# Kernel optimization log

Measured on AMD Instinct MI355X. Metric: run time of the kernel, lower is better.

Reference implementation:

```python
import jax, jax.numpy as jnp
import numpy as np

V = 10000   # vocab (input and output)
E = 128     # embed dim
H = 256     # hidden dim (encoder == decoder, required for shapes to work)
B = 64      # batch
S = 128     # src len
T = 64      # trg len


def setup_inputs() -> dict:
    key = jax.random.key(0)
    ks = jax.random.split(key, 24)
    sc = 0.05
    rn = lambda k, shp: jax.random.normal(k, shp, jnp.float32) * sc
    inp = {
        "src": jax.random.randint(ks[0], (B, S), 0, V),
        "trg": jax.random.randint(ks[1], (B, T), 0, V),
        "tf_mask": jnp.ones((T,), bool),  # True -> teacher forcing at that step
        # encoder params
        "enc_emb": rn(ks[2], (V, E)),
        "e1f_Wih": rn(ks[3], (4 * H, E)), "e1f_Whh": rn(ks[4], (4 * H, H)), "e1f_b": rn(ks[5], (4 * H,)),
        "e1b_Wih": rn(ks[6], (4 * H, E)), "e1b_Whh": rn(ks[7], (4 * H, H)), "e1b_b": rn(ks[8], (4 * H,)),
        "e2f_Wih": rn(ks[9], (4 * H, 2 * H)), "e2f_Whh": rn(ks[10], (4 * H, H)), "e2f_b": rn(ks[11], (4 * H,)),
        "e2b_Wih": rn(ks[12], (4 * H, 2 * H)), "e2b_Whh": rn(ks[13], (4 * H, H)), "e2b_b": rn(ks[14], (4 * H,)),
        # decoder params
        "dec_emb": rn(ks[15], (V, E)),
        "Wa": rn(ks[16], (H, 3 * H)), "ba": rn(ks[17], (H,)), "v": rn(ks[18], (H,)),
        "dWih": rn(ks[19], (4 * H, E + 2 * H)), "db": rn(ks[20], (4 * H,)),
        "Wfc": rn(ks[21], (V, 3 * H)), "bfc": rn(ks[22], (V,)),
    }
    return inp


def _lstm_dir(x, Wih, Whh, b, reverse):
    # x: [B, S, Din] -> hidden seq [B, S, H]; torch gate order i,f,g,o
    h0 = jnp.zeros((x.shape[0], Whh.shape[1]), x.dtype)

    def step(carry, xt):
        h, c = carry
        g = xt @ Wih.T + h @ Whh.T + b
        i, f, gg, o = jnp.split(g, 4, axis=-1)
        c = jax.nn.sigmoid(f) * c + jax.nn.sigmoid(i) * jnp.tanh(gg)
        h = jax.nn.sigmoid(o) * jnp.tanh(c)
        return (h, c), h

    _, hs = jax.lax.scan(step, (h0, h0), jnp.swapaxes(x, 0, 1), reverse=reverse)
    return jnp.swapaxes(hs, 0, 1)


def _bilstm(x, fW, fU, fb, bW, bU, bb):
    return jnp.concatenate([_lstm_dir(x, fW, fU, fb, False),
                            _lstm_dir(x, bW, bU, bb, True)], axis=-1)


def _seq2seq(src, trg, tf_mask, enc_emb,
             e1f_Wih, e1f_Whh, e1f_b, e1b_Wih, e1b_Whh, e1b_b,
             e2f_Wih, e2f_Whh, e2f_b, e2b_Wih, e2b_Whh, e2b_b,
             dec_emb, Wa, ba, v, dWih, db, Wfc, bfc):
    # encoder (dropout in eval mode -> identity)
    emb = enc_emb[src]                                   # [B,S,E]
    out1 = _bilstm(emb, e1f_Wih, e1f_Whh, e1f_b, e1b_Wih, e1b_Whh, e1b_b)   # [B,S,2H]
    enc_out = _bilstm(out1, e2f_Wih, e2f_Whh, e2f_b, e2b_Wih, e2b_Whh, e2b_b)  # [B,S,2H]

    bsz, slen = src.shape
    hidden0 = enc_out[:, -1, :H]                         # forward final state [B,H]

    def step(carry, xs):
        hidden, tok = carry
        trg_t, tf = xs
        embedded = dec_emb[tok]                          # [B,E]
        # Bahdanau attention
        rep = jnp.broadcast_to(hidden[:, None, :], (bsz, slen, H))
        energy = jnp.tanh(jnp.concatenate([rep, enc_out], -1) @ Wa.T + ba)  # [B,S,H]
        attn = jax.nn.softmax(energy @ v, axis=-1)       # [B,S]
        context = jnp.einsum('bs,bsd->bd', attn, enc_out)  # [B,2H]
        # LSTM step with fresh zero (h,c), as in the original (no state threaded)
        xin = jnp.concatenate([embedded, context], -1)   # [B,E+2H]
        g = xin @ dWih.T + db
        i, f, gg, o = jnp.split(g, 4, axis=-1)
        c = jax.nn.sigmoid(i) * jnp.tanh(gg)             # f gate irrelevant with c0=0
        h = jax.nn.sigmoid(o) * jnp.tanh(c)
        pred = jnp.concatenate([h, context], -1) @ Wfc.T + bfc  # [B,V]
        top1 = jnp.argmax(pred, axis=-1)
        nxt = jnp.where(tf, trg_t, top1)
        return (h, nxt), pred

    xs = (jnp.swapaxes(trg[:, 1:], 0, 1), tf_mask[1:])
    _, preds = jax.lax.scan(step, (hidden0, trg[:, 0]), xs)  # [T-1,B,V]
    preds = jnp.swapaxes(preds, 0, 1)                        # [B,T-1,V]
    zero0 = jnp.zeros((bsz, 1, preds.shape[-1]), preds.dtype)
    return jnp.concatenate([zero0, preds], axis=1)           # [B,T,V]


def reference(src, trg, tf_mask, enc_emb,
              e1f_Wih, e1f_Whh, e1f_b, e1b_Wih, e1b_Whh, e1b_b,
              e2f_Wih, e2f_Whh, e2f_b, e2b_Wih, e2b_Whh, e2b_b,
              dec_emb, Wa, ba, v, dWih, db, Wfc, bfc):
    return _seq2seq(src, trg, tf_mask, enc_emb,
                    e1f_Wih, e1f_Whh, e1f_b, e1b_Wih, e1b_Whh, e1b_b,
                    e2f_Wih, e2f_Whh, e2f_b, e2b_Wih, e2b_Whh, e2b_b,
                    dec_emb, Wa, ba, v, dWih, db, Wfc, bfc)
```

## Files before the change

### kernel.cpp

```cpp
#include <hip/hip_runtime.h>
#include <hip/hip_bf16.h>
#include <cstdint>


typedef __hip_bfloat16 bf16;
typedef __attribute__((ext_vector_type(8))) short short8;
typedef __attribute__((ext_vector_type(4))) float f32x4;

#define OFF_E1F_WIH 0L
#define OFF_E1B_WIH 131072L
#define OFF_E2F_WIH 262144L
#define OFF_E2B_WIH 786432L
#define OFF_E1F_WHH 1310720L
#define OFF_E1B_WHH 1572864L
#define OFF_E2F_WHH 1835008L
#define OFF_E2B_WHH 2097152L
#define OFF_DWIH    2359296L
#define OFF_WFC     3014656L
#define OFF_WA      10694656L
#define WBF_TOTAL   10891264L

__device__ __align__(16) bf16     g_WBF[WBF_TOTAL];
__device__ __align__(16) float    g_X1F[8192 * 1024];
__device__ __align__(16) float    g_X1B[8192 * 1024];
__device__ __align__(16) bf16     g_EMB[8192 * 128];
__device__ __align__(16) bf16     g_OUT1[8192 * 512];
__device__ __align__(16) bf16     g_ENC[8192 * 512];
__device__ __align__(16) float    g_EWA[8192 * 256];
__device__ __align__(16) float    g_HID[64 * 256];
__device__ __align__(16) bf16     g_XIN[64 * 640];
__device__ __align__(16) bf16     g_HC[64 * 768];

__device__ __forceinline__ float b2f(bf16 x) { return __bfloat162float(x); }
__device__ __forceinline__ float fexp2(float x) { return __builtin_amdgcn_exp2f(x); }
__device__ __forceinline__ float frcp(float x)  { return __builtin_amdgcn_rcpf(x); }
__device__ __forceinline__ float clampf(float x, float L) {
  return fminf(fmaxf(x, -L), L);
}
__device__ __forceinline__ float sigf(float x) {
  x = clampf(x, 30.f);
  return frcp(1.f + fexp2(-1.44269504f * x));
}
__device__ __forceinline__ float tanh_f(float x) {
  x = clampf(x, 15.f);
  float e = fexp2(2.885390082f * x);
  return (e - 1.f) * frcp(e + 1.f);
}
__device__ __forceinline__ f32x4 mfma16(short8 a, short8 b, f32x4 c) {
  return __builtin_amdgcn_mfma_f32_16x16x32_bf16(a, b, c, 0, 0, 0);
}

__global__ __launch_bounds__(256) void cvt_w(const float* __restrict__ src,
                                             long off, int n) {
  int i = (blockIdx.x * 256 + threadIdx.x) * 4;
  if (i >= n) return;
  float4 v = *(const float4*)(src + i);
  bf16* d = g_WBF + off + i;
  d[0] = __float2bfloat16(v.x);
  d[1] = __float2bfloat16(v.y);
  d[2] = __float2bfloat16(v.z);
  d[3] = __float2bfloat16(v.w);
}

__global__ __launch_bounds__(256) void embed_k(const int* __restrict__ src,
                                               const float* __restrict__ tab) {
  int i4 = (blockIdx.x * 256 + threadIdx.x) * 4;
  int row = i4 >> 7, e = i4 & 127;
  int tok = src[row];
  if (tok < 0 || tok >= 10000) tok = 0;
  float4 v = *(const float4*)&tab[(size_t)tok * 128 + e];
  bf16* d = &g_EMB[(size_t)row * 128 + e];
  d[0] = __float2bfloat16(v.x);
  d[1] = __float2bfloat16(v.y);
  d[2] = __float2bfloat16(v.z);
  d[3] = __float2bfloat16(v.w);
}

__device__ __forceinline__ void gemm_core(const bf16* __restrict__ A, int lda,
                                          const bf16* __restrict__ W, int ldw, int wcol,
                                          const float* __restrict__ bias,
                                          float* __restrict__ Cf,
                                          long ldc, int N, int K, float clampL) {
  const int wave = threadIdx.x >> 6, lane = threadIdx.x & 63;
  const int l15 = lane & 15, quad = lane >> 4;
  const int m0 = blockIdx.x * 64 + wave * 16;
  const int n0 = blockIdx.y * 64;

  f32x4 acc[4];
#pragma unroll
  for (int j = 0; j < 4; ++j) acc[j] = (f32x4){0.f, 0.f, 0.f, 0.f};

  const bf16* Arow = A + (size_t)(m0 + l15) * lda + quad * 8;
  for (int k = 0; k < K; k += 32) {
    short8 a = *(const short8*)(Arow + k);
#pragma unroll
    for (int j = 0; j < 4; ++j) {
      int n = n0 + 16 * j + l15;
      short8 bfr = (short8){0, 0, 0, 0, 0, 0, 0, 0};
      if (n < N) bfr = *(const short8*)(W + (size_t)n * ldw + wcol + k + quad * 8);
      acc[j] = mfma16(a, bfr, acc[j]);
    }
  }
#pragma unroll
  for (int j = 0; j < 4; ++j) {
    int n = n0 + 16 * j + l15;
    if (n >= N) continue;
    float bv = bias ? bias[n] : 0.f;
#pragma unroll
    for (int r = 0; r < 4; ++r) {
      int m = m0 + quad * 4 + r;
      Cf[(size_t)m * ldc + n] = clampf(acc[j][r] + bv, clampL);
    }
  }
}

__global__ __launch_bounds__(256) void gemm_x1(long offW, const float* __restrict__ bias,
                                               int bwd) {
  gemm_core(g_EMB, 128, g_WBF + offW, 128, 0, bias, bwd ? g_X1B : g_X1F,
            1024, 1024, 128, 64.f);
}
__global__ __launch_bounds__(256) void gemm_x2(long offW, const float* __restrict__ bias,
                                               int bwd) {
  gemm_core(g_OUT1, 512, g_WBF + offW, 512, 0, bias, bwd ? g_X1B : g_X1F,
            1024, 1024, 512, 64.f);
}
__global__ __launch_bounds__(256) void gemm_ewa() {
  gemm_core(g_ENC, 512, g_WBF + OFF_WA, 768, 256, nullptr, g_EWA, 256, 256, 512, 64.f);
}
__global__ __launch_bounds__(256) void gemm_pred(const float* __restrict__ bfc,
                                                 float* __restrict__ outp, int step) {
  gemm_core(g_HC, 768, g_WBF + OFF_WFC, 768, 0, bfc, outp + (size_t)step * 10000,
            640000, 10000, 768, 512.f);
}

__global__ __launch_bounds__(512, 2) void lstm_batch(long offWhf, long offWhb,
                                                     int layer) {
  const int bx = blockIdx.x;
  const int d = bx & 1, bg = bx >> 1;
  const int b0 = bg * 16;
  const float* __restrict__ X  = d ? g_X1B : g_X1F;
  const bf16*  __restrict__ Wh = g_WBF + (d ? offWhb : offWhf);
  bf16* __restrict__ out = layer ? g_ENC : g_OUT1;

  __shared__ __align__(16) bf16 hlds[16 * 264];
  __shared__ float gst[16 * 1028];

  const int tid = threadIdx.x;
  const int wave = tid >> 6, lane = tid & 63, l15 = lane & 15, quad = lane >> 4;
  const int n0 = wave * 128;
  const int u  = tid & 255;
  const int bh = tid >> 8;

  short8 bs[4][8];
#pragma unroll
  for (int kt = 0; kt < 4; ++kt)
#pragma unroll
    for (int nt = 0; nt < 8; ++nt)
      bs[kt][nt] = *(const short8*)(Wh + (size_t)(n0 + 16 * nt + l15) * 256 +
                                    kt * 32 + quad * 8);

  for (int i = tid; i < 16 * 264; i += 512) hlds[i] = __float2bfloat16(0.f);
  float creg[8];
#pragma unroll
  for (int i = 0; i < 8; ++i) creg[i] = 0.f;

  float xreg[32];
  {
    const int s0 = d ? 127 : 0;
#pragma unroll
    for (int j = 0; j < 8; ++j) {
      const size_t xr = ((size_t)(b0 + bh * 8 + j) * 128 + s0) * 1024 + u;
#pragma unroll
      for (int g = 0; g < 4; ++g) xreg[j * 4 + g] = X[xr + g * 256];
    }
  }
  __syncthreads();

  const bf16* Wstr = Wh + (size_t)(n0 + l15) * 256 + quad * 8;

  for (int t = 0; t < 128; ++t) {
    const int s = d ? (127 - t) : t;
    f32x4 acc[8];
#pragma unroll
    for (int nt = 0; nt < 8; ++nt) acc[nt] = (f32x4){0.f, 0.f, 0.f, 0.f};

#pragma unroll
    for (int kt = 0; kt < 4; ++kt) {
      short8 a = *(const short8*)&hlds[l15 * 264 + kt * 32 + quad * 8];
#pragma unroll
      for (int nt = 0; nt < 8; ++nt) acc[nt] = mfma16(a, bs[kt][nt], acc[nt]);
    }
#pragma unroll
    for (int kt = 4; kt < 8; ++kt) {
      short8 a = *(const short8*)&hlds[l15 * 264 + kt * 32 + quad * 8];
#pragma unroll
      for (int nt = 0; nt < 8; ++nt) {
        short8 bfr = *(const short8*)(Wstr + (size_t)nt * 16 * 256 + kt * 32);
        acc[nt] = mfma16(a, bfr, acc[nt]);
      }
    }

#pragma unroll
    for (int nt = 0; nt < 8; ++nt) {
      int col = n0 + 16 * nt + l15;
#pragma unroll
      for (int r = 0; r < 4; ++r)
        gst[(quad * 4 + r) * 1028 + col] = clampf(acc[nt][r], 64.f);
    }
    __syncthreads();

#pragma unroll
    for (int j = 0; j < 8; ++j) {
      const int b = bh * 8 + j;
      const int gb = b0 + b;
      float gi = gst[b * 1028 + u]       + xreg[j * 4 + 0];
      float gf = gst[b * 1028 + 256 + u] + xreg[j * 4 + 1];
      float gg = gst[b * 1028 + 512 + u] + xreg[j * 4 + 2];
      float go = gst[b * 1028 + 768 + u] + xreg[j * 4 + 3];
      float c = clampf(sigf(gf) * creg[j] + sigf(gi) * tanh_f(gg), 256.f);
      creg[j] = c;
      float h = clampf(sigf(go) * tanh_f(c), 4.f);
      out[((size_t)gb * 128 + s) * 512 + (size_t)d * 256 + u] = __float2bfloat16(h);
      if (layer == 1 && d == 0 && t == 127)
        g_HID[gb * 256 + u] = h;
      hlds[b * 264 + u] = __float2bfloat16(h);
    }

    {
      const int tn = (t < 127) ? (t + 1) : t;
      const int sn = d ? (127 - tn) : tn;
#pragma unroll
      for (int j = 0; j < 8; ++j) {
        const size_t xr = ((size_t)(b0 + bh * 8 + j) * 128 + sn) * 1024 + u;
#pragma unroll
        for (int g = 0; g < 4; ++g) xreg[j * 4 + g] = X[xr + g * 256];
      }
    }
    __syncthreads();
  }
}

__global__ __launch_bounds__(256) void attn_step(int step,
                                                 const int* __restrict__ trg,
                                                 const unsigned char* __restrict__ tfm,
                                                 const float* __restrict__ dec_emb,
                                                 const float* __restrict__ Wa,
                                                 const float* __restrict__ ba,
                                                 const float* __restrict__ vv,
                                                 const float* __restrict__ outp)
{
  int b = blockIdx.x, tid = threadIdx.x;
  __shared__ float sh[256], hb[256], vsh[256], es[128], red[256];
  __shared__ int ridx[256];
  __shared__ int stok;

  if (step == 1) {
    if (tid == 0) stok = trg[b * 64];
  } else {
    const float* pr = outp + (size_t)b * 640000 + (size_t)(step - 1) * 10000;
    float bv = -3.4e38f; int bi = 0;
    for (int v2 = tid; v2 < 10000; v2 += 256) {
      float pv = pr[v2];
      if (pv > bv) { bv = pv; bi = v2; }
    }
    red[tid] = bv; ridx[tid] = bi;
    __syncthreads();
    for (int off = 128; off; off >>= 1) {
      if (tid < off) {
        float ov = red[tid + off]; int oi = ridx[tid + off];
        if (ov > red[tid] || (ov == red[tid] && oi < ridx[tid])) { red[tid] = ov; ridx[tid] = oi; }
      }
      __syncthreads();
    }
    if (tid == 0) {
      int k = step - 1;
      int tf = (int)tfm[k] | (int)tfm[4 * k];
      int tok = tf ? trg[b * 64 + k] : ridx[0];
      if (tok < 0 || tok >= 10000) tok = 0;
      stok = tok;
    }
    __syncthreads();
  }

  sh[tid]  = g_HID[b * 256 + tid];
  vsh[tid] = vv[tid];
  __syncthreads();

  {
    float acc = 0.f;
    const float* wr = Wa + (size_t)tid * 768;
    for (int k4 = 0; k4 < 256; k4 += 4) {
      float4 w4 = *(const float4*)(wr + k4);
      acc += sh[k4] * w4.x + sh[k4 + 1] * w4.y + sh[k4 + 2] * w4.z + sh[k4 + 3] * w4.w;
    }
    hb[tid] = clampf(acc + ba[tid], 64.f);
  }
  __syncthreads();

  int wv = tid >> 6, ln = tid & 63;
  for (int s = wv; s < 128; s += 4) {
    const float* Er = g_EWA + ((size_t)b * 128 + s) * 256;
    float part = 0.f;
#pragma unroll
    for (int jj = 0; jj < 4; ++jj) {
      int j = ln + 64 * jj;
      part += tanh_f(hb[j] + Er[j]) * vsh[j];
    }
    part += __shfl_down(part, 32);
    part += __shfl_down(part, 16);
    part += __shfl_down(part, 8);
    part += __shfl_down(part, 4);
    part += __shfl_down(part, 2);
    part += __shfl_down(part, 1);
    if (ln == 0) es[s] = clampf(part, 512.f);
  }
  __syncthreads();

  red[tid] = (tid < 128) ? es[tid] : -3.4e38f;
  __syncthreads();
  for (int off = 128; off; off >>= 1) { if (tid < off) red[tid] = fmaxf(red[tid], red[tid + off]); __syncthreads(); }
  float mx = red[0];
  __syncthreads();
  float pexp = (tid < 128) ? fexp2((es[tid] - mx) * 1.44269504f) : 0.f;
  red[tid] = pexp;
  __syncthreads();
  for (int off = 128; off; off >>= 1) { if (tid < off) red[tid] += red[tid + off]; __syncthreads(); }
  float inv = frcp(red[0]);
  __syncthreads();
  if (tid < 128) es[tid] = pexp * inv;
  __syncthreads();

  float c0 = 0.f, c1 = 0.f;
  for (int s = 0; s < 128; ++s) {
    const bf16* er = g_ENC + ((size_t)b * 128 + s) * 512;
    float a = es[s];
    c0 += a * b2f(er[tid]);
    c1 += a * b2f(er[tid + 256]);
  }
  c0 = clampf(c0, 16.f);
  c1 = clampf(c1, 16.f);
  g_XIN[(size_t)b * 640 + 128 + tid] = __float2bfloat16(c0);
  g_XIN[(size_t)b * 640 + 384 + tid] = __float2bfloat16(c1);
  g_HC [(size_t)b * 768 + 256 + tid] = __float2bfloat16(c0);
  g_HC [(size_t)b * 768 + 512 + tid] = __float2bfloat16(c1);
  if (tid < 128)
    g_XIN[(size_t)b * 640 + tid] = __float2bfloat16(dec_emb[(size_t)stok * 128 + tid]);
}

__global__ __launch_bounds__(256) void dec_gemm_cell(const float* __restrict__ db) {
  __shared__ float gst[64 * 68];
  const int tid = threadIdx.x;
  const int wave = tid >> 6, lane = tid & 63, l15 = lane & 15, quad = lane >> 4;
  const int u0 = blockIdx.x * 16;

  f32x4 acc[4];
#pragma unroll
  for (int mt = 0; mt < 4; ++mt) acc[mt] = (f32x4){0.f, 0.f, 0.f, 0.f};

  const bf16* Brow = g_WBF + OFF_DWIH + (size_t)(wave * 256 + u0 + l15) * 640 + quad * 8;
  for (int kt = 0; kt < 20; ++kt) {
    short8 bfr = *(const short8*)(Brow + kt * 32);
#pragma unroll
    for (int mt = 0; mt < 4; ++mt) {
      short8 a = *(const short8*)(g_XIN + (size_t)(16 * mt + l15) * 640 + kt * 32 + quad * 8);
      acc[mt] = mfma16(a, bfr, acc[mt]);
    }
  }
#pragma unroll
  for (int mt = 0; mt < 4; ++mt)
#pragma unroll
    for (int r = 0; r < 4; ++r)
      gst[(16 * mt + quad * 4 + r) * 68 + wave * 16 + l15] = clampf(acc[mt][r], 64.f);
  __syncthreads();

  for (int p = tid; p < 1024; p += 256) {
    int b = p >> 4, uu = p & 15;
    int u = u0 + uu;
    float gi = gst[b * 68 + 0  + uu] + db[u];
    float gg = gst[b * 68 + 32 + uu] + db[512 + u];
    float go = gst[b * 68 + 48 + uu] + db[768 + u];
    float c = sigf(gi) * tanh_f(gg);
    float h = clampf(sigf(go) * tanh_f(c), 4.f);
    g_HID[b * 256 + u] = h;
    g_HC[(size_t)b * 768 + u] = __float2bfloat16(h);
  }
}

__global__ __launch_bounds__(256) void zero_t0(float* __restrict__ outp) {
  int idx = blockIdx.x * 256 + threadIdx.x;
  int b = idx / 10000, v = idx - b * 10000;
  outp[(size_t)b * 640000 + v] = 0.f;
}

extern "C" void kernel_launch(void* const* d_in, const int* in_sizes, int n_in,
                              void* d_out, int out_size, void* d_ws, size_t ws_size,
                              hipStream_t stream) {
  (void)in_sizes; (void)n_in; (void)out_size; (void)d_ws; (void)ws_size;

  const int*   src     = (const int*)   d_in[0];
  const int*   trg     = (const int*)   d_in[1];
  const unsigned char* tfm = (const unsigned char*) d_in[2];
  const float* enc_emb = (const float*) d_in[3];
  const float* e1f_Wih = (const float*) d_in[4];
  const float* e1f_Whh = (const float*) d_in[5];
  const float* e1f_b   = (const float*) d_in[6];
  const float* e1b_Wih = (const float*) d_in[7];
  const float* e1b_Whh = (const float*) d_in[8];
  const float* e1b_b   = (const float*) d_in[9];
  const float* e2f_Wih = (const float*) d_in[10];
  const float* e2f_Whh = (const float*) d_in[11];
  const float* e2f_b   = (const float*) d_in[12];
  const float* e2b_Wih = (const float*) d_in[13];
  const float* e2b_Whh = (const float*) d_in[14];
  const float* e2b_b   = (const float*) d_in[15];
  const float* dec_emb = (const float*) d_in[16];
  const float* Wa      = (const float*) d_in[17];
  const float* ba      = (const float*) d_in[18];
  const float* vv      = (const float*) d_in[19];
  const float* dWih    = (const float*) d_in[20];
  const float* db      = (const float*) d_in[21];
  const float* Wfc     = (const float*) d_in[22];
  const float* bfc     = (const float*) d_in[23];
  float* outp = (float*) d_out;

  cvt_w<<<128,  256, 0, stream>>>(e1f_Wih, OFF_E1F_WIH, 131072);
  cvt_w<<<128,  256, 0, stream>>>(e1b_Wih, OFF_E1B_WIH, 131072);
  cvt_w<<<512,  256, 0, stream>>>(e2f_Wih, OFF_E2F_WIH, 524288);
  cvt_w<<<512,  256, 0, stream>>>(e2b_Wih, OFF_E2B_WIH, 524288);
  cvt_w<<<256,  256, 0, stream>>>(e1f_Whh, OFF_E1F_WHH, 262144);
  cvt_w<<<256,  256, 0, stream>>>(e1b_Whh, OFF_E1B_WHH, 262144);
  cvt_w<<<256,  256, 0, stream>>>(e2f_Whh, OFF_E2F_WHH, 262144);
  cvt_w<<<256,  256, 0, stream>>>(e2b_Whh, OFF_E2B_WHH, 262144);
  cvt_w<<<640,  256, 0, stream>>>(dWih,    OFF_DWIH,    655360);
  cvt_w<<<7500, 256, 0, stream>>>(Wfc,     OFF_WFC,     7680000);
  cvt_w<<<192,  256, 0, stream>>>(Wa,      OFF_WA,      196608);

  embed_k<<<1024, 256, 0, stream>>>(src, enc_emb);
  gemm_x1<<<dim3(128, 16), 256, 0, stream>>>(OFF_E1F_WIH, e1f_b, 0);
  gemm_x1<<<dim3(128, 16), 256, 0, stream>>>(OFF_E1B_WIH, e1b_b, 1);
  lstm_batch<<<8, 512, 0, stream>>>(OFF_E1F_WHH, OFF_E1B_WHH, 0);
  gemm_x2<<<dim3(128, 16), 256, 0, stream>>>(OFF_E2F_WIH, e2f_b, 0);
  gemm_x2<<<dim3(128, 16), 256, 0, stream>>>(OFF_E2B_WIH, e2b_b, 1);
  lstm_batch<<<8, 512, 0, stream>>>(OFF_E2F_WHH, OFF_E2B_WHH, 1);
  gemm_ewa<<<dim3(128, 4), 256, 0, stream>>>();
  zero_t0<<<2500, 256, 0, stream>>>(outp);

  for (int i = 1; i < 64; ++i) {
    attn_step<<<64, 256, 0, stream>>>(i, trg, tfm, dec_emb, Wa, ba, vv, outp);
    dec_gemm_cell<<<16, 256, 0, stream>>>(db);
    gemm_pred<<<dim3(1, 157), 256, 0, stream>>>(bfc, outp, i);
  }
}
```

Measured before the change: 9.436 ms.

## Fuse LSTM gate math in registers, interleave X gates, stage Whh in LDS

The recurrent LSTM kernel now permutes the Whh column assignment so that each wave's MFMA accumulators hold all four gates for the same hidden units. The cell update therefore runs directly from registers, and the shared gate staging buffer and one barrier per step go away. The input-projection GEMMs write gates interleaved per unit so each thread reads one float4 instead of four scattered floats. Part of Whh (k-tiles 4-5) is cached in LDS, and the h buffer is double-buffered. The cost is more LDS use, which may reduce occupancy.

```diff
diff --git a/kernel.cpp b/kernel.cpp
--- a/kernel.cpp
+++ b/kernel.cpp
@@ -80,7 +80,8 @@
                                           const bf16* __restrict__ W, int ldw, int wcol,
                                           const float* __restrict__ bias,
                                           float* __restrict__ Cf,
-                                          long ldc, int N, int K, float clampL) {
+                                          long ldc, int N, int K, float clampL,
+                                          int xg) {
   const int wave = threadIdx.x >> 6, lane = threadIdx.x & 63;
   const int l15 = lane & 15, quad = lane >> 4;
   const int m0 = blockIdx.x * 64 + wave * 16;
@@ -109,7 +110,9 @@
 #pragma unroll
     for (int r = 0; r < 4; ++r) {
       int m = m0 + quad * 4 + r;
-      Cf[(size_t)m * ldc + n] = clampf(acc[j][r] + bv, clampL);
+      size_t idx = xg ? ((size_t)m * 1024 + (size_t)(n & 255) * 4 + (n >> 8))
+                      : ((size_t)m * ldc + n);
+      Cf[idx] = clampf(acc[j][r] + bv, clampL);
     }
   }
 }
@@ -117,20 +120,21 @@
 __global__ __launch_bounds__(256) void gemm_x1(long offW, const float* __restrict__ bias,
                                                int bwd) {
   gemm_core(g_EMB, 128, g_WBF + offW, 128, 0, bias, bwd ? g_X1B : g_X1F,
-            1024, 1024, 128, 64.f);
+            1024, 1024, 128, 64.f, 1);
 }
 __global__ __launch_bounds__(256) void gemm_x2(long offW, const float* __restrict__ bias,
                                                int bwd) {
   gemm_core(g_OUT1, 512, g_WBF + offW, 512, 0, bias, bwd ? g_X1B : g_X1F,
-            1024, 1024, 512, 64.f);
+            1024, 1024, 512, 64.f, 1);
 }
 __global__ __launch_bounds__(256) void gemm_ewa() {
-  gemm_core(g_ENC, 512, g_WBF + OFF_WA, 768, 256, nullptr, g_EWA, 256, 256, 512, 64.f);
+  gemm_core(g_ENC, 512, g_WBF + OFF_WA, 768, 256, nullptr, g_EWA, 256, 256, 512,
+            64.f, 0);
 }
 __global__ __launch_bounds__(256) void gemm_pred(const float* __restrict__ bfc,
                                                  float* __restrict__ outp, int step) {
   gemm_core(g_HC, 768, g_WBF + OFF_WFC, 768, 0, bfc, outp + (size_t)step * 10000,
-            640000, 10000, 768, 512.f);
+            640000, 10000, 768, 512.f, 0);
 }
 
 __global__ __launch_bounds__(512, 2) void lstm_batch(long offWhf, long offWhb,
@@ -142,42 +146,62 @@
   const bf16*  __restrict__ Wh = g_WBF + (d ? offWhb : offWhf);
   bf16* __restrict__ out = layer ? g_ENC : g_OUT1;
 
-  __shared__ __align__(16) bf16 hlds[16 * 264];
-  __shared__ float gst[16 * 1028];
+  __shared__ __align__(16) bf16 hlds[2][16 * 264];
+  __shared__ __align__(16) bf16 wlds[8192 * 8];
 
   const int tid = threadIdx.x;
   const int wave = tid >> 6, lane = tid & 63, l15 = lane & 15, quad = lane >> 4;
-  const int n0 = wave * 128;
-  const int u  = tid & 255;
-  const int bh = tid >> 8;
 
   short8 bs[4][8];
 #pragma unroll
-  for (int kt = 0; kt < 4; ++kt)
-#pragma unroll
-    for (int nt = 0; nt < 8; ++nt)
-      bs[kt][nt] = *(const short8*)(Wh + (size_t)(n0 + 16 * nt + l15) * 256 +
+  for (int nt = 0; nt < 8; ++nt) {
+    const int colbase = (nt >> 1) * 256 + 32 * wave + 16 * (nt & 1);
+#pragma unroll
+    for (int kt = 0; kt < 4; ++kt)
+      bs[kt][nt] = *(const short8*)(Wh + (size_t)(colbase + l15) * 256 +
                                     kt * 32 + quad * 8);
-
-  for (int i = tid; i < 16 * 264; i += 512) hlds[i] = __float2bfloat16(0.f);
+  }
+
+  for (int it = 0; it < 16; ++it) {
+    const int uid = tid * 16 + it;
+    const int l = uid & 63, kt2 = (uid >> 6) & 1;
+    const int nt = (uid >> 7) & 7, w = uid >> 10;
+    const int colbase = (nt >> 1) * 256 + 32 * w + 16 * (nt & 1);
+    short8 v = *(const short8*)(Wh + (size_t)(colbase + (l & 15)) * 256 +
+                                (4 + kt2) * 32 + (l >> 4) * 8);
+    *(short8*)&wlds[(size_t)uid * 8] = v;
+  }
+
+  const bf16* Wrow[8];
+#pragma unroll
+  for (int nt = 0; nt < 8; ++nt) {
+    const int colbase = (nt >> 1) * 256 + 32 * wave + 16 * (nt & 1);
+    Wrow[nt] = Wh + (size_t)(colbase + l15) * 256 + quad * 8;
+  }
+
+  for (int i = tid; i < 2 * 16 * 264; i += 512)
+    ((bf16*)hlds)[i] = __float2bfloat16(0.f);
+
   float creg[8];
 #pragma unroll
   for (int i = 0; i < 8; ++i) creg[i] = 0.f;
 
-  float xreg[32];
+  float4 xg[8];
   {
     const int s0 = d ? 127 : 0;
 #pragma unroll
-    for (int j = 0; j < 8; ++j) {
-      const size_t xr = ((size_t)(b0 + bh * 8 + j) * 128 + s0) * 1024 + u;
-#pragma unroll
-      for (int g = 0; g < 4; ++g) xreg[j * 4 + g] = X[xr + g * 256];
-    }
-  }
-  __syncthreads();
-
-  const bf16* Wstr = Wh + (size_t)(n0 + l15) * 256 + quad * 8;
-
+    for (int h2 = 0; h2 < 2; ++h2) {
+      const int u = 32 * wave + 16 * h2 + l15;
+#pragma unroll
+      for (int r = 0; r < 4; ++r) {
+        const int gb = b0 + quad * 4 + r;
+        xg[h2 * 4 + r] = *(const float4*)&X[(((size_t)gb * 128 + s0) * 256 + u) * 4];
+      }
+    }
+  }
+  __syncthreads();
+
+  int p = 0;
   for (int t = 0; t < 128; ++t) {
     const int s = d ? (127 - t) : t;
     f32x4 acc[8];
@@ -186,57 +210,64 @@
 
 #pragma unroll
     for (int kt = 0; kt < 4; ++kt) {
-      short8 a = *(const short8*)&hlds[l15 * 264 + kt * 32 + quad * 8];
+      short8 a = *(const short8*)&hlds[p][l15 * 264 + kt * 32 + quad * 8];
 #pragma unroll
       for (int nt = 0; nt < 8; ++nt) acc[nt] = mfma16(a, bs[kt][nt], acc[nt]);
     }
 #pragma unroll
-    for (int kt = 4; kt < 8; ++kt) {
-      short8 a = *(const short8*)&hlds[l15 * 264 + kt * 32 + quad * 8];
+    for (int kt2 = 0; kt2 < 2; ++kt2) {
+      short8 a = *(const short8*)&hlds[p][l15 * 264 + (4 + kt2) * 32 + quad * 8];
 #pragma unroll
       for (int nt = 0; nt < 8; ++nt) {
-        short8 bfr = *(const short8*)(Wstr + (size_t)nt * 16 * 256 + kt * 32);
+        short8 bfr = *(const short8*)&wlds[(size_t)(((wave * 8 + nt) * 2 + kt2) * 64 + lane) * 8];
         acc[nt] = mfma16(a, bfr, acc[nt]);
       }
     }
-
-#pragma unroll
-    for (int nt = 0; nt < 8; ++nt) {
-      int col = n0 + 16 * nt + l15;
-#pragma unroll
-      for (int r = 0; r < 4; ++r)
-        gst[(quad * 4 + r) * 1028 + col] = clampf(acc[nt][r], 64.f);
+#pragma unroll
+    for (int kt = 6; kt < 8; ++kt) {
+      short8 a = *(const short8*)&hlds[p][l15 * 264 + kt * 32 + quad * 8];
+#pragma unroll
+      for (int nt = 0; nt < 8; ++nt) {
+        short8 bfr = *(const short8*)(Wrow[nt] + kt * 32);
+        acc[nt] = mfma16(a, bfr, acc[nt]);
+      }
+    }
+
+#pragma unroll
+    for (int h2 = 0; h2 < 2; ++h2) {
+      const int u = 32 * wave + 16 * h2 + l15;
+#pragma unroll
+      for (int r = 0; r < 4; ++r) {
+        const int b = quad * 4 + r, gb = b0 + b, ci = h2 * 4 + r;
+        const float4 xv = xg[ci];
+        float gi = clampf(acc[0 + h2][r], 64.f) + xv.x;
+        float gf = clampf(acc[2 + h2][r], 64.f) + xv.y;
+        float gg = clampf(acc[4 + h2][r], 64.f) + xv.z;
+        float go = clampf(acc[6 + h2][r], 64.f) + xv.w;
+        float c = clampf(sigf(gf) * creg[ci] + sigf(gi) * tanh_f(gg), 256.f);
+        creg[ci] = c;
+        float h = clampf(sigf(go) * tanh_f(c), 4.f);
+        out[((size_t)gb * 128 + s) * 512 + (size_t)d * 256 + u] = __float2bfloat16(h);
+        if (layer == 1 && d == 0 && t == 127)
+          g_HID[gb * 256 + u] = h;
+        hlds[p ^ 1][b * 264 + u] = __float2bfloat16(h);
+      }
+    }
+
+    if (t < 127) {
+      const int sn = d ? (126 - t) : (t + 1);
+#pragma unroll
+      for (int h2 = 0; h2 < 2; ++h2) {
+        const int u = 32 * wave + 16 * h2 + l15;
+#pragma unroll
+        for (int r = 0; r < 4; ++r) {
+          const int gb = b0 + quad * 4 + r;
+          xg[h2 * 4 + r] = *(const float4*)&X[(((size_t)gb * 128 + sn) * 256 + u) * 4];
+        }
+      }
     }
     __syncthreads();
-
-#pragma unroll
-    for (int j = 0; j < 8; ++j) {
-      const int b = bh * 8 + j;
-      const int gb = b0 + b;
-      float gi = gst[b * 1028 + u]       + xreg[j * 4 + 0];
-      float gf = gst[b * 1028 + 256 + u] + xreg[j * 4 + 1];
-      float gg = gst[b * 1028 + 512 + u] + xreg[j * 4 + 2];
-      float go = gst[b * 1028 + 768 + u] + xreg[j * 4 + 3];
-      float c = clampf(sigf(gf) * creg[j] + sigf(gi) * tanh_f(gg), 256.f);
-      creg[j] = c;
-      float h = clampf(sigf(go) * tanh_f(c), 4.f);
-      out[((size_t)gb * 128 + s) * 512 + (size_t)d * 256 + u] = __float2bfloat16(h);
-      if (layer == 1 && d == 0 && t == 127)
-        g_HID[gb * 256 + u] = h;
-      hlds[b * 264 + u] = __float2bfloat16(h);
-    }
-
-    {
-      const int tn = (t < 127) ? (t + 1) : t;
-      const int sn = d ? (127 - tn) : tn;
-#pragma unroll
-      for (int j = 0; j < 8; ++j) {
-        const size_t xr = ((size_t)(b0 + bh * 8 + j) * 128 + sn) * 1024 + u;
-#pragma unroll
-        for (int g = 0; g < 4; ++g) xreg[j * 4 + g] = X[xr + g * 256];
-      }
-    }
-    __syncthreads();
+    p ^= 1;
   }
 }
 
```

Result: faster. 7.692 ms (-18.5%).
